# Kernel optimization log

Measured on AMD Instinct MI355X. Metric: run time of the kernel, lower is better.

Reference implementation:

```python
import jax, jax.numpy as jnp
import numpy as np

EMB = 300      # LEN_EMB_VECTOR
FH, FO = 200, 200
GH, GO = 200, 200
HH, HO = 200, 3

def _mlp2(x, w1, b1, w2, b2):
    # relu(Linear) -> relu(Linear), torch Linear: y = x @ W.T + b
    h = jax.nn.relu(x @ w1.T + b1)
    return jax.nn.relu(h @ w2.T + b2)

def setup_inputs() -> dict:
    key = jax.random.key(0)
    ks = jax.random.split(key, 16)
    L1, L2 = 8192, 8192
    def lin(k, out_d, in_d):
        kw, kb = jax.random.split(k)
        s = 1.0 / np.sqrt(in_d)
        w = jax.random.uniform(kw, (out_d, in_d), jnp.float32, -s, s)
        b = jax.random.uniform(kb, (out_d,), jnp.float32, -s, s)
        return w, b
    F_w1, F_b1 = lin(ks[0], FH, EMB)
    F_w2, F_b2 = lin(ks[1], FO, FH)
    G_w1, G_b1 = lin(ks[2], GH, 2 * EMB)
    G_w2, G_b2 = lin(ks[3], GO, GH)
    H_w1, H_b1 = lin(ks[4], HH, 2 * GO)
    H_w2, H_b2 = lin(ks[5], HO, HH)
    sen1 = jax.random.normal(ks[6], (L1, EMB), jnp.float32)
    sen2 = jax.random.normal(ks[7], (L2, EMB), jnp.float32)
    return {"sen1": sen1, "sen2": sen2,
            "F_w1": F_w1, "F_b1": F_b1, "F_w2": F_w2, "F_b2": F_b2,
            "G_w1": G_w1, "G_b1": G_b1, "G_w2": G_w2, "G_b2": G_b2,
            "H_w1": H_w1, "H_b1": H_b1, "H_w2": H_w2, "H_b2": H_b2}

def reference(sen1, sen2, F_w1, F_b1, F_w2, F_b2,
              G_w1, G_b1, G_w2, G_b2, H_w1, H_b1, H_w2, H_b2):
    # F projection of every token in both sentences
    Fa = _mlp2(sen1, F_w1, F_b1, F_w2, F_b2)   # [L1, 200]
    Fb = _mlp2(sen2, F_w1, F_b1, F_w2, F_b2)   # [L2, 200]
    # E matrix of dot products: e_ij = Fa_i . Fb_j
    E = jnp.einsum('id,jd->ij', Fa, Fb)        # [L1, L2]
    # beta_i = softmax over j of E[i, :] applied to sen2
    beta = jax.nn.softmax(E, axis=1) @ sen2    # [L1, EMB]
    # alpha_j = softmax over i of E[:, j] applied to sen1
    alpha = jax.nn.softmax(E, axis=0).T @ sen1 # [L2, EMB]
    # G comparison
    v1 = _mlp2(jnp.concatenate([sen1, beta], axis=-1), G_w1, G_b1, G_w2, G_b2)   # [L1, 200]
    v2 = _mlp2(jnp.concatenate([sen2, alpha], axis=-1), G_w1, G_b1, G_w2, G_b2)  # [L2, 200]
    # aggregate: elementwise sums over tokens, then H classifier with softmax
    hx = jnp.concatenate([v1.sum(axis=0), v2.sum(axis=0)])  # [400]
    logits = jax.nn.relu(hx @ H_w1.T + H_b1) @ H_w2.T + H_b2  # [3]
    return jax.nn.softmax(logits)
```

## Files before the change

### kernel.cpp

```cpp
#include <hip/hip_runtime.h>

typedef __attribute__((ext_vector_type(8))) short short8;
typedef __attribute__((ext_vector_type(4))) float f32x4;

__device__ inline ushort f2bf(float f) {
    union { float f; unsigned u; } v{f};
    unsigned r = v.u + 0x7FFF + ((v.u >> 16) & 1);
    return (ushort)(r >> 16);
}
__device__ inline float bf2f(ushort u) {
    union { unsigned u; float f; } v;
    v.u = ((unsigned)u) << 16;
    return v.f;
}

__device__ inline void gload_lds16(const void* g, void* l) {
    __builtin_amdgcn_global_load_lds(
        (const __attribute__((address_space(1))) unsigned int*)(uintptr_t)g,
        (__attribute__((address_space(3))) unsigned int*)(uintptr_t)l,
        16, 0, 0);
}

__global__ __launch_bounds__(256) void convert_sen_kernel(
    const float* __restrict__ s1, const float* __restrict__ s2,
    ushort* __restrict__ Senb, ushort* __restrict__ St1, ushort* __restrict__ St2)
{
    const float* X = blockIdx.z ? s2 : s1;
    ushort* Xt = blockIdx.z ? St2 : St1;
    ushort* Sb = Senb + (size_t)blockIdx.z * 8192 * 320;
    __shared__ float t[64][65];
    const int r0 = blockIdx.x * 64, c0 = blockIdx.y * 64;
    const int tc = threadIdx.x & 63, tr = threadIdx.x >> 6;
    for (int rr = tr; rr < 64; rr += 4) {
        int c = c0 + tc;
        float v = (c < 300) ? X[(size_t)(r0 + rr) * 300 + c] : 0.f;
        t[rr][tc] = v;
        if (c < 320) Sb[(size_t)(r0 + rr) * 320 + c] = f2bf(v);
    }
    __syncthreads();
    for (int rr = tr; rr < 64; rr += 4) {
        int oc = c0 + rr;
        if (oc < 320)
            Xt[(size_t)oc * 8192 + r0 + tc] = f2bf(t[tc][rr]);
    }
}

__global__ __launch_bounds__(256) void convert_weights_kernel(
    const float* __restrict__ W0, const float* __restrict__ b0,
    const float* __restrict__ W1, const float* __restrict__ b1,
    const float* __restrict__ W2, const float* __restrict__ b2,
    const float* __restrict__ W3, const float* __restrict__ b3,
    ushort* __restrict__ Wb0, float* __restrict__ bp0,
    ushort* __restrict__ Wb1, float* __restrict__ bp1,
    ushort* __restrict__ Wb2, float* __restrict__ bp2,
    ushort* __restrict__ Wb3, float* __restrict__ bp3)
{
    const int id = blockIdx.x;
    const int mat = id / 224, n = id % 224;
    if (mat == 2) {
        for (int k = threadIdx.x; k < 640; k += 256) {
            float v = 0.f;
            if (n < 200) {
                if (k < 320) { if (k < 300) v = W2[(size_t)n * 600 + k]; }
                else { int cc = k - 320; if (cc < 300) v = W2[(size_t)n * 600 + 300 + cc]; }
            }
            Wb2[(size_t)n * 640 + k] = f2bf(v);
        }
        if (threadIdx.x == 0) bp2[n] = (n < 200) ? b2[n] : 0.f;
        return;
    }
    const float* W; const float* b; ushort* Wb; float* bp; int N, K, KP;
    if (mat == 0)      { W = W0; b = b0; Wb = Wb0; bp = bp0; N = 200; K = 300; KP = 320; }
    else if (mat == 1) { W = W1; b = b1; Wb = Wb1; bp = bp1; N = 200; K = 200; KP = 224; }
    else               { W = W3; b = b3; Wb = Wb3; bp = bp3; N = 200; K = 200; KP = 224; }
    for (int k = threadIdx.x; k < KP; k += 256)
        Wb[(size_t)n * KP + k] = (n < N && k < K) ? f2bf(W[(size_t)n * K + k]) : (ushort)0;
    if (threadIdx.x == 0) bp[n] = (n < N) ? b[n] : 0.f;
}

__global__ __launch_bounds__(64) void mlp2_kernel(
    const ushort* __restrict__ X, int KP1,
    const ushort* __restrict__ W1, const float* __restrict__ b1,
    const ushort* __restrict__ W2, const float* __restrict__ b2,
    ushort* __restrict__ Ybf)
{
    const int r0 = blockIdx.x * 16;
    const int lane = threadIdx.x;
    const int lr = lane & 15, lg = lane >> 4;

    __shared__ __align__(16) ushort Y1[16][232];

    f32x4 a1[14];
#pragma unroll
    for (int t = 0; t < 14; ++t) a1[t] = f32x4{0.f, 0.f, 0.f, 0.f};

    const ushort* Xrow = X + (size_t)(r0 + lr) * KP1 + lg * 8;
    const ushort* W1r  = W1 + (size_t)lr * KP1 + lg * 8;
    for (int k0 = 0; k0 < KP1; k0 += 32) {
        short8 a = *(const short8*)(Xrow + k0);
#pragma unroll
        for (int t = 0; t < 14; ++t) {
            short8 bfr = *(const short8*)(W1r + (size_t)t * 16 * KP1 + k0);
            a1[t] = __builtin_amdgcn_mfma_f32_16x16x32_bf16(a, bfr, a1[t], 0, 0, 0);
        }
    }
#pragma unroll
    for (int t = 0; t < 14; ++t) {
        int col = t * 16 + lr;
        float bv = b1[col];
#pragma unroll
        for (int rr = 0; rr < 4; ++rr)
            Y1[lg * 4 + rr][col] = f2bf(fmaxf(a1[t][rr] + bv, 0.f));
    }
    __syncthreads();

    f32x4 a2[14];
#pragma unroll
    for (int t = 0; t < 14; ++t) a2[t] = f32x4{0.f, 0.f, 0.f, 0.f};
    const ushort* W2r = W2 + (size_t)lr * 224 + lg * 8;
    for (int k0 = 0; k0 < 224; k0 += 32) {
        short8 a = *(const short8*)&Y1[lr][lg * 8 + k0];
#pragma unroll
        for (int t = 0; t < 14; ++t) {
            short8 bfr = *(const short8*)(W2r + (size_t)t * 16 * 224 + k0);
            a2[t] = __builtin_amdgcn_mfma_f32_16x16x32_bf16(a, bfr, a2[t], 0, 0, 0);
        }
    }
#pragma unroll
    for (int t = 0; t < 14; ++t) {
        int col = t * 16 + lr;
        float bv = b2[col];
#pragma unroll
        for (int rr = 0; rr < 4; ++rr) {
            int row = r0 + lg * 4 + rr;
            Ybf[(size_t)row * 224 + col] = f2bf(fmaxf(a2[t][rr] + bv, 0.f));
        }
    }
}

__global__ __launch_bounds__(64) void gmlp2_kernel(
    const ushort* __restrict__ Senb,
    const float* __restrict__ Pacc, const float* __restrict__ Dpart,
    const ushort* __restrict__ W1, const float* __restrict__ b1,
    const ushort* __restrict__ W2, const float* __restrict__ b2,
    ushort* __restrict__ v)
{
    const int r0 = blockIdx.x * 16;
    const int lane = threadIdx.x;
    const int lr = lane & 15, lg = lane >> 4;
    const int row = r0 + lr;

    __shared__ __align__(16) ushort Y1[16][232];

    const float inv = 1.f / (Dpart[row] + Dpart[16384 + row]);
    const float* pa = Pacc + (size_t)row * 320;
    const float* pb = pa + (size_t)16384 * 320;

    f32x4 a1[14];
#pragma unroll
    for (int t = 0; t < 14; ++t) a1[t] = f32x4{0.f, 0.f, 0.f, 0.f};

    const ushort* Xrow = Senb + (size_t)row * 320 + lg * 8;
    const ushort* W1r  = W1 + (size_t)lr * 640 + lg * 8;
    for (int k0 = 0; k0 < 640; k0 += 32) {
        short8 a;
        if (k0 < 320) {
            a = *(const short8*)(Xrow + k0);
        } else {
            int kk = k0 - 320 + lg * 8;
            float4 x0 = *(const float4*)(pa + kk);
            float4 x1 = *(const float4*)(pa + kk + 4);
            float4 y0 = *(const float4*)(pb + kk);
            float4 y1 = *(const float4*)(pb + kk + 4);
            a[0] = (short)f2bf((x0.x + y0.x) * inv);
            a[1] = (short)f2bf((x0.y + y0.y) * inv);
            a[2] = (short)f2bf((x0.z + y0.z) * inv);
            a[3] = (short)f2bf((x0.w + y0.w) * inv);
            a[4] = (short)f2bf((x1.x + y1.x) * inv);
            a[5] = (short)f2bf((x1.y + y1.y) * inv);
            a[6] = (short)f2bf((x1.z + y1.z) * inv);
            a[7] = (short)f2bf((x1.w + y1.w) * inv);
        }
#pragma unroll
        for (int t = 0; t < 14; ++t) {
            short8 bfr = *(const short8*)(W1r + (size_t)t * 16 * 640 + k0);
            a1[t] = __builtin_amdgcn_mfma_f32_16x16x32_bf16(a, bfr, a1[t], 0, 0, 0);
        }
    }
#pragma unroll
    for (int t = 0; t < 14; ++t) {
        int col = t * 16 + lr;
        float bv = b1[col];
#pragma unroll
        for (int rr = 0; rr < 4; ++rr)
            Y1[lg * 4 + rr][col] = f2bf(fmaxf(a1[t][rr] + bv, 0.f));
    }
    __syncthreads();

    f32x4 a2[14];
#pragma unroll
    for (int t = 0; t < 14; ++t) a2[t] = f32x4{0.f, 0.f, 0.f, 0.f};
    const ushort* W2r = W2 + (size_t)lr * 224 + lg * 8;
    for (int k0 = 0; k0 < 224; k0 += 32) {
        short8 a = *(const short8*)&Y1[lr][lg * 8 + k0];
#pragma unroll
        for (int t = 0; t < 14; ++t) {
            short8 bfr = *(const short8*)(W2r + (size_t)t * 16 * 224 + k0);
            a2[t] = __builtin_amdgcn_mfma_f32_16x16x32_bf16(a, bfr, a2[t], 0, 0, 0);
        }
    }
#pragma unroll
    for (int t = 0; t < 14; ++t) {
        int col = t * 16 + lr;
        if (col < 200) {
            float bv = b2[col];
#pragma unroll
            for (int rr = 0; rr < 4; ++rr) {
                int orow = r0 + lg * 4 + rr;
                v[(size_t)orow * 200 + col] = f2bf(fmaxf(a2[t][rr] + bv, 0.f));
            }
        }
    }
}

__global__ __launch_bounds__(512, 2) void attend_mfma_kernel(
    const ushort* __restrict__ FaFb, const ushort* __restrict__ St1,
    const ushort* __restrict__ St2, float* __restrict__ Pacc,
    float* __restrict__ Dpart)
{
    const int b = blockIdx.x;
    const int it  = b & 63;
    const int jh  = (b >> 6) & 1;
    const int dir = b >> 7;
    const ushort* A  = FaFb + (dir ? (size_t)8192 * 224 : 0);
    const ushort* B  = FaFb + (dir ? 0 : (size_t)8192 * 224);
    const ushort* St = dir ? St1 : St2;
    const int ib = it * 128;
    const int jo = jh * 4096;

    const int tid = threadIdx.x;
    const int w = tid >> 6;
    const int wi = w >> 1, wj = w & 1;
    const int dq = w & 3,  ih = w >> 2;
    const int lane = tid & 63;
    const int lr = lane & 15, lg = lane >> 4;

    __shared__ __align__(16) ushort Bl[2][28 * 512];
    __shared__ __align__(16) ushort Sl[2][40 * 512];
    __shared__ __align__(16) ushort Pl[128][76];
    __shared__ float dled[8][32];

    f32x4 acc[4][5];
#pragma unroll
    for (int s = 0; s < 4; ++s)
#pragma unroll
        for (int t = 0; t < 5; ++t) acc[s][t] = f32x4{0.f, 0.f, 0.f, 0.f};
    float dsum[2] = {0.f, 0.f};

    short8 afr[2][7];
#pragma unroll
    for (int si = 0; si < 2; ++si) {
        const ushort* Ar = A + (size_t)(ib + wi * 32 + si * 16 + lr) * 224 + lg * 8;
#pragma unroll
        for (int k = 0; k < 7; ++k) afr[si][k] = *(const short8*)(Ar + k * 32);
    }

    const int nB = (w < 4) ? 4 : 3;
    const int pB = (w < 4) ? (w * 4) : (16 + (w - 4) * 3);
    int boff[4];
#pragma unroll
    for (int q = 0; q < 4; ++q) {
        int p = pB + q;
        boff[q] = ((p / 7) * 16 + lr) * 448 + ((p % 7) * 32 + lg * 8) * 2;
    }
    const char* Bb = (const char*)B + (size_t)jo * 448;

    int soff[5];
#pragma unroll
    for (int q = 0; q < 5; ++q) {
        int p = w * 5 + q;
        int srow = p * 8 + (lane >> 3);
        int sl = (lane & 7) ^ (srow & 7);
        soff[q] = srow * 16384 + sl * 16;
    }
    const char* Sb = (const char*)St + (size_t)jo * 2;

    int prow[5], prow7[5];
#pragma unroll
    for (int t = 0; t < 5; ++t) {
        prow[t] = (dq * 80 + t * 16 + lr) * 128;
        prow7[t] = (dq * 80 + t * 16 + lr) & 7;
    }

#pragma unroll
    for (int q = 0; q < 4; ++q)
        if (q < nB) gload_lds16(Bb + boff[q], &Bl[0][(pB + q) * 512]);
#pragma unroll
    for (int q = 0; q < 5; ++q)
        gload_lds16(Sb + soff[q], &Sl[0][(w * 5 + q) * 512]);
    __syncthreads();

    int buf = 0;
    for (int jb = 0; jb < 4096; jb += 64, buf ^= 1) {
        f32x4 e[2][2];
#pragma unroll
        for (int si = 0; si < 2; ++si)
#pragma unroll
            for (int jt = 0; jt < 2; ++jt) e[si][jt] = f32x4{0.f, 0.f, 0.f, 0.f};
        __builtin_amdgcn_s_setprio(1);
#pragma unroll
        for (int kk = 0; kk < 7; ++kk) {
            short8 b0 = *(const short8*)&Bl[buf][((2 * wj + 0) * 7 + kk) * 512 + lane * 8];
            short8 b1 = *(const short8*)&Bl[buf][((2 * wj + 1) * 7 + kk) * 512 + lane * 8];
            e[0][0] = __builtin_amdgcn_mfma_f32_16x16x32_bf16(b0, afr[0][kk], e[0][0], 0, 0, 0);
            e[1][0] = __builtin_amdgcn_mfma_f32_16x16x32_bf16(b0, afr[1][kk], e[1][0], 0, 0, 0);
            e[0][1] = __builtin_amdgcn_mfma_f32_16x16x32_bf16(b1, afr[0][kk], e[0][1], 0, 0, 0);
            e[1][1] = __builtin_amdgcn_mfma_f32_16x16x32_bf16(b1, afr[1][kk], e[1][1], 0, 0, 0);
        }
        __builtin_amdgcn_s_setprio(0);

#pragma unroll
        for (int si = 0; si < 2; ++si) {
#pragma unroll
            for (int jt = 0; jt < 2; ++jt) {
                float x0 = __expf(e[si][jt][0]);
                float x1 = __expf(e[si][jt][1]);
                float x2 = __expf(e[si][jt][2]);
                float x3 = __expf(e[si][jt][3]);
                dsum[si] += (x0 + x1) + (x2 + x3);
                uint2 pk;
                pk.x = (unsigned)f2bf(x0) | ((unsigned)f2bf(x1) << 16);
                pk.y = (unsigned)f2bf(x2) | ((unsigned)f2bf(x3) << 16);
                *(uint2*)&Pl[wi * 32 + si * 16 + lr][wj * 32 + jt * 16 + lg * 4] = pk;
            }
        }
        __syncthreads();

        if (jb + 64 < 4096) {
            const char* Bn = Bb + (size_t)(jb + 64) * 448;
            const char* Sn = Sb + (size_t)(jb + 64) * 2;
#pragma unroll
            for (int q = 0; q < 4; ++q)
                if (q < nB) gload_lds16(Bn + boff[q], &Bl[buf ^ 1][(pB + q) * 512]);
#pragma unroll
            for (int q = 0; q < 5; ++q)
                gload_lds16(Sn + soff[q], &Sl[buf ^ 1][(w * 5 + q) * 512]);
        }

#pragma unroll
        for (int h = 0; h < 2; ++h) {
            short8 pf[4];
#pragma unroll
            for (int s = 0; s < 4; ++s)
                pf[s] = *(const short8*)&Pl[ih * 64 + s * 16 + lr][h * 32 + lg * 8];
            short8 st[5];
#pragma unroll
            for (int t = 0; t < 5; ++t) {
                int sl = ((h << 2) | lg) ^ prow7[t];
                st[t] = *(const short8*)((const char*)Sl[buf] + prow[t] + (sl << 4));
            }
            __builtin_amdgcn_s_setprio(1);
#pragma unroll
            for (int s = 0; s < 4; ++s)
#pragma unroll
                for (int t = 0; t < 5; ++t)
                    acc[s][t] = __builtin_amdgcn_mfma_f32_16x16x32_bf16(pf[s], st[t], acc[s][t], 0, 0, 0);
            __builtin_amdgcn_s_setprio(0);
        }
        __syncthreads();
    }

#pragma unroll
    for (int si = 0; si < 2; ++si) {
        dsum[si] += __shfl_xor(dsum[si], 16);
        dsum[si] += __shfl_xor(dsum[si], 32);
    }
    if (lg == 0) {
#pragma unroll
        for (int si = 0; si < 2; ++si)
            dled[w][si * 16 + lr] = dsum[si];
    }
    __syncthreads();

    if (tid < 128) {
        int wi2 = tid >> 5, idx = tid & 31;
        Dpart[(size_t)jh * 16384 + dir * 8192 + ib + tid] =
            dled[wi2 * 2][idx] + dled[wi2 * 2 + 1][idx];
    }

    float* Pb = Pacc + ((size_t)jh * 16384 + dir * 8192 + ib + ih * 64) * 320;
#pragma unroll
    for (int t = 0; t < 5; ++t) {
        int d = dq * 80 + t * 16 + lr;
#pragma unroll
        for (int s = 0; s < 4; ++s)
#pragma unroll
            for (int r = 0; r < 4; ++r)
                Pb[(size_t)(s * 16 + lg * 4 + r) * 320 + d] = acc[s][t][r];
    }
}

__global__ __launch_bounds__(256) void colsum_kernel(
    const ushort* __restrict__ v, float* __restrict__ hsum)
{
    const int c = blockIdx.x;
    const ushort* V = v + (c < 200 ? 0 : (size_t)8192 * 200);
    const int col = c % 200;
    float s = 0.f;
    for (int r = threadIdx.x; r < 8192; r += 256)
        s += bf2f(V[(size_t)r * 200 + col]);
    __shared__ float red[256];
    red[threadIdx.x] = s;
    __syncthreads();
    for (int off = 128; off > 0; off >>= 1) {
        if (threadIdx.x < off) red[threadIdx.x] += red[threadIdx.x + off];
        __syncthreads();
    }
    if (threadIdx.x == 0) hsum[c] = red[0];
}

__global__ __launch_bounds__(256) void head_kernel(
    const float* __restrict__ hsum,
    const float* __restrict__ Hw1, const float* __restrict__ Hb1,
    const float* __restrict__ Hw2, const float* __restrict__ Hb2,
    float* __restrict__ out)
{
    __shared__ float hx[400];
    __shared__ float hr[200];
    __shared__ float lg[3];
    const int t = threadIdx.x;
    for (int i = t; i < 400; i += 256) hx[i] = hsum[i];
    __syncthreads();
    if (t < 200) {
        float a = Hb1[t];
        for (int k = 0; k < 400; ++k) a = fmaf(hx[k], Hw1[t * 400 + k], a);
        hr[t] = fmaxf(a, 0.f);
    }
    __syncthreads();
    if (t < 3) {
        float a = Hb2[t];
        for (int k = 0; k < 200; ++k) a = fmaf(hr[k], Hw2[t * 200 + k], a);
        lg[t] = a;
    }
    __syncthreads();
    if (t == 0) {
        float m = fmaxf(lg[0], fmaxf(lg[1], lg[2]));
        float e0 = __expf(lg[0] - m);
        float e1 = __expf(lg[1] - m);
        float e2 = __expf(lg[2] - m);
        float s = e0 + e1 + e2;
        out[0] = e0 / s;
        out[1] = e1 / s;
        out[2] = e2 / s;
    }
}

extern "C" void kernel_launch(void* const* d_in, const int* in_sizes, int n_in,
                              void* d_out, int out_size, void* d_ws, size_t ws_size,
                              hipStream_t stream)
{
    const float* sen1 = (const float*)d_in[0];
    const float* sen2 = (const float*)d_in[1];
    const float* F_w1 = (const float*)d_in[2];
    const float* F_b1 = (const float*)d_in[3];
    const float* F_w2 = (const float*)d_in[4];
    const float* F_b2 = (const float*)d_in[5];
    const float* G_w1 = (const float*)d_in[6];
    const float* G_b1 = (const float*)d_in[7];
    const float* G_w2 = (const float*)d_in[8];
    const float* G_b2 = (const float*)d_in[9];
    const float* H_w1 = (const float*)d_in[10];
    const float* H_b1 = (const float*)d_in[11];
    const float* H_w2 = (const float*)d_in[12];
    const float* H_b2 = (const float*)d_in[13];
    float* out = (float*)d_out;

    const int L = 8192;
    char* p = (char*)d_ws;
    ushort* St1  = (ushort*)p; p += (size_t)320 * L * 2;
    ushort* St2  = (ushort*)p; p += (size_t)320 * L * 2;
    ushort* Senb = (ushort*)p; p += (size_t)2 * L * 320 * 2;
    ushort* FaFb = (ushort*)p; p += (size_t)2 * L * 224 * 2;
    ushort* vbuf = (ushort*)p; p += (size_t)2 * L * 200 * 2;
    ushort* WbF1 = (ushort*)p; p += (size_t)224 * 320 * 2;
    ushort* WbF2 = (ushort*)p; p += (size_t)224 * 224 * 2;
    ushort* WbG1 = (ushort*)p; p += (size_t)224 * 640 * 2;
    ushort* WbG2 = (ushort*)p; p += (size_t)224 * 224 * 2;
    float*  bpF1 = (float*)p;  p += 224 * 4;
    float*  bpF2 = (float*)p;  p += 224 * 4;
    float*  bpG1 = (float*)p;  p += 224 * 4;
    float*  bpG2 = (float*)p;  p += 224 * 4;
    float*  hsum = (float*)p;  p += 400 * 4;
    float*  Pacc = (float*)p;  p += (size_t)2 * 16384 * 320 * 4;
    float*  Dpart= (float*)p;  p += (size_t)2 * 16384 * 4;

    dim3 blk256(256);

    hipLaunchKernelGGL(convert_sen_kernel, dim3(L / 64, 5, 2), blk256, 0, stream,
                       sen1, sen2, Senb, St1, St2);
    hipLaunchKernelGGL(convert_weights_kernel, dim3(4 * 224), blk256, 0, stream,
                       F_w1, F_b1, F_w2, F_b2, G_w1, G_b1, G_w2, G_b2,
                       WbF1, bpF1, WbF2, bpF2, WbG1, bpG1, WbG2, bpG2);

    hipLaunchKernelGGL(mlp2_kernel, dim3(2 * L / 16), dim3(64), 0, stream,
                       Senb, 320, WbF1, bpF1, WbF2, bpF2, FaFb);

    hipLaunchKernelGGL(attend_mfma_kernel, dim3(256), dim3(512), 0, stream,
                       FaFb, St1, St2, Pacc, Dpart);

    hipLaunchKernelGGL(gmlp2_kernel, dim3(2 * L / 16), dim3(64), 0, stream,
                       Senb, Pacc, Dpart, WbG1, bpG1, WbG2, bpG2, vbuf);

    hipLaunchKernelGGL(colsum_kernel, dim3(400), blk256, 0, stream, vbuf, hsum);
    hipLaunchKernelGGL(head_kernel, dim3(1), blk256, 0, stream,
                       hsum, H_w1, H_b1, H_w2, H_b2, out);
}
```

Before: 295.1 us.

## Store attention partials in bf16 and fuse G-MLP column sums into gmlp2

The attention kernel now writes its unnormalized partial context sums as bf16 instead of fp32, halving the Pacc write and read traffic between the attend and G-MLP kernels. The gmlp2 kernel no longer writes per-token outputs. It reduces each 16-row block across lanes and writes one partial column sum per block, so the final colsum kernel only has to reduce 512 partials per column instead of scanning 8192 strided rows. This risks some accuracy because the partial sums are rounded to bf16 before the two halves are combined and normalized.

```diff
diff --git a/kernel.cpp b/kernel.cpp
--- a/kernel.cpp
+++ b/kernel.cpp
@@ -140,10 +140,10 @@
 
 __global__ __launch_bounds__(64) void gmlp2_kernel(
     const ushort* __restrict__ Senb,
-    const float* __restrict__ Pacc, const float* __restrict__ Dpart,
+    const ushort* __restrict__ Pacc, const float* __restrict__ Dpart,
     const ushort* __restrict__ W1, const float* __restrict__ b1,
     const ushort* __restrict__ W2, const float* __restrict__ b2,
-    ushort* __restrict__ v)
+    float* __restrict__ Part)
 {
     const int r0 = blockIdx.x * 16;
     const int lane = threadIdx.x;
@@ -153,8 +153,8 @@
     __shared__ __align__(16) ushort Y1[16][232];
 
     const float inv = 1.f / (Dpart[row] + Dpart[16384 + row]);
-    const float* pa = Pacc + (size_t)row * 320;
-    const float* pb = pa + (size_t)16384 * 320;
+    const ushort* pa = Pacc + (size_t)row * 320;
+    const ushort* pb = pa + (size_t)16384 * 320;
 
     f32x4 a1[14];
 #pragma unroll
@@ -168,18 +168,11 @@
             a = *(const short8*)(Xrow + k0);
         } else {
             int kk = k0 - 320 + lg * 8;
-            float4 x0 = *(const float4*)(pa + kk);
-            float4 x1 = *(const float4*)(pa + kk + 4);
-            float4 y0 = *(const float4*)(pb + kk);
-            float4 y1 = *(const float4*)(pb + kk + 4);
-            a[0] = (short)f2bf((x0.x + y0.x) * inv);
-            a[1] = (short)f2bf((x0.y + y0.y) * inv);
-            a[2] = (short)f2bf((x0.z + y0.z) * inv);
-            a[3] = (short)f2bf((x0.w + y0.w) * inv);
-            a[4] = (short)f2bf((x1.x + y1.x) * inv);
-            a[5] = (short)f2bf((x1.y + y1.y) * inv);
-            a[6] = (short)f2bf((x1.z + y1.z) * inv);
-            a[7] = (short)f2bf((x1.w + y1.w) * inv);
+            short8 x = *(const short8*)(pa + kk);
+            short8 y = *(const short8*)(pb + kk);
+#pragma unroll
+            for (int m = 0; m < 8; ++m)
+                a[m] = (short)f2bf((bf2f((ushort)x[m]) + bf2f((ushort)y[m])) * inv);
         }
 #pragma unroll
         for (int t = 0; t < 14; ++t) {
@@ -214,18 +207,21 @@
         int col = t * 16 + lr;
         if (col < 200) {
             float bv = b2[col];
-#pragma unroll
-            for (int rr = 0; rr < 4; ++rr) {
-                int orow = r0 + lg * 4 + rr;
-                v[(size_t)orow * 200 + col] = f2bf(fmaxf(a2[t][rr] + bv, 0.f));
-            }
+            float s = 0.f;
+#pragma unroll
+            for (int rr = 0; rr < 4; ++rr)
+                s += fmaxf(a2[t][rr] + bv, 0.f);
+            s += __shfl_xor(s, 16);
+            s += __shfl_xor(s, 32);
+            if (lg == 0)
+                Part[(size_t)blockIdx.x * 200 + col] = s;
         }
     }
 }
 
 __global__ __launch_bounds__(512, 2) void attend_mfma_kernel(
     const ushort* __restrict__ FaFb, const ushort* __restrict__ St1,
-    const ushort* __restrict__ St2, float* __restrict__ Pacc,
+    const ushort* __restrict__ St2, ushort* __restrict__ Pacc,
     float* __restrict__ Dpart)
 {
     const int b = blockIdx.x;
@@ -388,7 +384,7 @@
             dled[wi2 * 2][idx] + dled[wi2 * 2 + 1][idx];
     }
 
-    float* Pb = Pacc + ((size_t)jh * 16384 + dir * 8192 + ib + ih * 64) * 320;
+    ushort* Pb = Pacc + ((size_t)jh * 16384 + dir * 8192 + ib + ih * 64) * 320;
 #pragma unroll
     for (int t = 0; t < 5; ++t) {
         int d = dq * 80 + t * 16 + lr;
@@ -396,19 +392,19 @@
         for (int s = 0; s < 4; ++s)
 #pragma unroll
             for (int r = 0; r < 4; ++r)
-                Pb[(size_t)(s * 16 + lg * 4 + r) * 320 + d] = acc[s][t][r];
-    }
-}
-
-__global__ __launch_bounds__(256) void colsum_kernel(
-    const ushort* __restrict__ v, float* __restrict__ hsum)
+                Pb[(size_t)(s * 16 + lg * 4 + r) * 320 + d] = f2bf(acc[s][t][r]);
+    }
+}
+
+__global__ __launch_bounds__(256) void colsum_part_kernel(
+    const float* __restrict__ Part, float* __restrict__ hsum)
 {
     const int c = blockIdx.x;
-    const ushort* V = v + (c < 200 ? 0 : (size_t)8192 * 200);
+    const int base = (c < 200) ? 0 : 512;
     const int col = c % 200;
     float s = 0.f;
-    for (int r = threadIdx.x; r < 8192; r += 256)
-        s += bf2f(V[(size_t)r * 200 + col]);
+    for (int p = threadIdx.x; p < 512; p += 256)
+        s += Part[(size_t)(base + p) * 200 + col];
     __shared__ float red[256];
     red[threadIdx.x] = s;
     __syncthreads();
@@ -481,7 +477,6 @@
     ushort* St2  = (ushort*)p; p += (size_t)320 * L * 2;
     ushort* Senb = (ushort*)p; p += (size_t)2 * L * 320 * 2;
     ushort* FaFb = (ushort*)p; p += (size_t)2 * L * 224 * 2;
-    ushort* vbuf = (ushort*)p; p += (size_t)2 * L * 200 * 2;
     ushort* WbF1 = (ushort*)p; p += (size_t)224 * 320 * 2;
     ushort* WbF2 = (ushort*)p; p += (size_t)224 * 224 * 2;
     ushort* WbG1 = (ushort*)p; p += (size_t)224 * 640 * 2;
@@ -491,8 +486,9 @@
     float*  bpG1 = (float*)p;  p += 224 * 4;
     float*  bpG2 = (float*)p;  p += 224 * 4;
     float*  hsum = (float*)p;  p += 400 * 4;
-    float*  Pacc = (float*)p;  p += (size_t)2 * 16384 * 320 * 4;
+    ushort* Pacc = (ushort*)p; p += (size_t)2 * 16384 * 320 * 2;
     float*  Dpart= (float*)p;  p += (size_t)2 * 16384 * 4;
+    float*  Part = (float*)p;  p += (size_t)1024 * 200 * 4;
 
     dim3 blk256(256);
 
@@ -509,9 +505,9 @@
                        FaFb, St1, St2, Pacc, Dpart);
 
     hipLaunchKernelGGL(gmlp2_kernel, dim3(2 * L / 16), dim3(64), 0, stream,
-                       Senb, Pacc, Dpart, WbG1, bpG1, WbG2, bpG2, vbuf);
-
-    hipLaunchKernelGGL(colsum_kernel, dim3(400), blk256, 0, stream, vbuf, hsum);
+                       Senb, Pacc, Dpart, WbG1, bpG1, WbG2, bpG2, Part);
+
+    hipLaunchKernelGGL(colsum_part_kernel, dim3(400), blk256, 0, stream, Part, hsum);
     hipLaunchKernelGGL(head_kernel, dim3(1), blk256, 0, stream,
                        hsum, H_w1, H_b1, H_w2, H_b2, out);
 }
```

Measured after the change: 275.9 us, median of 2. 1.07x faster.
